# Optimization experiments

Measured on AMD Instinct MI355X. Metric: run time of the kernel, lower is better.

## Reference

```python
import jax, jax.numpy as jnp
import numpy as np

B, S, C, H = 2, 4096, 640, 8
D = C // H  # head_dim = 80


def setup_inputs() -> dict:
    key = jax.random.key(0)
    ks = jax.random.split(key, 5)
    init = 0.02
    return {
        "hidden_states": jax.random.normal(ks[0], (B, S, C), dtype=jnp.float32),
        "Wq": jax.random.normal(ks[1], (C, C), dtype=jnp.float32) * init,
        "Wk": jax.random.normal(ks[2], (C, C), dtype=jnp.float32) * init,
        "Wv": jax.random.normal(ks[3], (C, C), dtype=jnp.float32) * init,
        "Wo": jax.random.normal(ks[4], (C, C), dtype=jnp.float32) * init,
        "bo": jnp.zeros((C,), dtype=jnp.float32),
    }


def reference(hidden_states, Wq, Wk, Wv, Wo, bo):
    # self-attention: encoder_hidden_states is None -> k,v from hidden_states
    x = hidden_states  # [B, S, C]
    q = jnp.einsum("bsc,cd->bsd", x, Wq)
    k = jnp.einsum("bsc,cd->bsd", x, Wk)
    v = jnp.einsum("bsc,cd->bsd", x, Wv)

    # head_to_batch_dim: [B, S, H*D] -> [B, H, S, D]
    def split_heads(t):
        return t.reshape(B, S, H, D).transpose(0, 2, 1, 3)

    q, k, v = split_heads(q), split_heads(k), split_heads(v)

    scale = 1.0 / jnp.sqrt(jnp.float32(D))
    # get_attention_scores: baddbmm(q, k^T) * scale, softmax over keys
    scores = jnp.einsum("bhqd,bhkd->bhqk", q, k) * scale  # [B, H, S, S]
    probs = jax.nn.softmax(scores, axis=-1)
    out = jnp.einsum("bhqk,bhkd->bhqd", probs, v)  # [B, H, S, D]

    # batch_to_head_dim + to_out[0] linear (Dropout is identity at eval)
    out = out.transpose(0, 2, 1, 3).reshape(B, S, C)
    out = jnp.einsum("bsc,cd->bsd", out, Wo) + bo
    # residual_connection=False, rescale_output_factor=1.0 (diffusers defaults)
    return out
```

## Files before the change

kernel.cpp:

```cpp
#include <hip/hip_runtime.h>
#include <hip/hip_bf16.h>

typedef __bf16 bf16x8 __attribute__((ext_vector_type(8)));
typedef float f32x4 __attribute__((ext_vector_type(4)));
typedef float f32x16 __attribute__((ext_vector_type(16)));
typedef unsigned short u16;
typedef unsigned int u32;
typedef u16 u16x8 __attribute__((ext_vector_type(8)));

#define DEV __device__ __forceinline__

DEV u16 f2b(float f) {
    u32 u = __builtin_bit_cast(u32, f);
    u32 r = (u + 0x7FFFu + ((u >> 16) & 1u)) >> 16;
    return (u16)r;
}
DEV bf16x8 load8(const u16* p) {
    return __builtin_bit_cast(bf16x8, *(const uint4*)p);
}
DEV u32 cvtpk(float lo, float hi) {
    u32 r;
    asm("v_cvt_pk_bf16_f32 %0, %1, %2" : "=v"(r) : "v"(lo), "v"(hi));
    return r;
}
DEV void gld_lds16(const u16* g, const char* l) {
    __builtin_amdgcn_global_load_lds(
        (const __attribute__((address_space(1))) u32*)(unsigned long long)g,
        (__attribute__((address_space(3))) u32*)(u32)(unsigned long long)l,
        16, 0, 0);
}

__global__ __launch_bounds__(256) void cvt_x(const float* __restrict__ X, u16* __restrict__ Xb) {
    long i = ((long)blockIdx.x * 256 + threadIdx.x) * 8;
    float fa[8];
    *(uint4*)fa = *(const uint4*)(X + i);
    *(uint4*)(fa + 4) = *(const uint4*)(X + i + 4);
    u16x8 t;
    #pragma unroll
    for (int j = 0; j < 8; ++j) t[j] = f2b(fa[j]);
    *(u16x8*)(Xb + i) = t;
}

__global__ __launch_bounds__(256) void cvt_w3(
    const float* __restrict__ Wq, const float* __restrict__ Wk, const float* __restrict__ Wv,
    u16* __restrict__ Wt3)
{
    const int z = blockIdx.z;
    const float* W = (z == 0) ? Wq : ((z == 1) ? Wk : Wv);
    u16* Wt = Wt3 + (long)z * 409600;
    const int k0 = blockIdx.x * 64, n0 = blockIdx.y * 64;
    const int t = threadIdx.x;
    __shared__ u16 T[64][72];
    {
        int kl = t >> 2, nc = (t & 3) * 16;
        const float* src = W + (long)(k0 + kl) * 640 + n0 + nc;
        float fa[16];
        #pragma unroll
        for (int i = 0; i < 4; ++i) *(uint4*)(fa + i * 4) = *(const uint4*)(src + i * 4);
        #pragma unroll
        for (int j = 0; j < 16; ++j) T[nc + j][kl] = f2b(fa[j]);
    }
    __syncthreads();
    {
        int nl = t >> 2, kc = (t & 3) * 16;
        u16* dst = Wt + (long)(n0 + nl) * 640 + k0 + kc;
        *(uint4*)dst = *(const uint4*)&T[nl][kc];
        *(uint4*)(dst + 8) = *(const uint4*)&T[nl][kc + 8];
    }
}
__global__ __launch_bounds__(256) void cvt_w1(const float* __restrict__ W, u16* __restrict__ Wt) {
    const int k0 = blockIdx.x * 64, n0 = blockIdx.y * 64;
    const int t = threadIdx.x;
    __shared__ u16 T[64][72];
    {
        int kl = t >> 2, nc = (t & 3) * 16;
        const float* src = W + (long)(k0 + kl) * 640 + n0 + nc;
        float fa[16];
        #pragma unroll
        for (int i = 0; i < 4; ++i) *(uint4*)(fa + i * 4) = *(const uint4*)(src + i * 4);
        #pragma unroll
        for (int j = 0; j < 16; ++j) T[nc + j][kl] = f2b(fa[j]);
    }
    __syncthreads();
    {
        int nl = t >> 2, kc = (t & 3) * 16;
        u16* dst = Wt + (long)(n0 + nl) * 640 + k0 + kc;
        *(uint4*)dst = *(const uint4*)&T[nl][kc];
        *(uint4*)(dst + 8) = *(const uint4*)&T[nl][kc + 8];
    }
}

#define GEMM_CORE(A_PTR, BT_PTR)                                                  \
    const int tid = threadIdx.x;                                                  \
    const int lane = tid & 63;                                                    \
    const int w = tid >> 6;                                                       \
    const int wm = w >> 1, wn = w & 1;                                            \
    const int lg = lane >> 4, lr = lane & 15;                                     \
    __shared__ __align__(16) char Bb[2][16384];                                   \
    auto stage = [&](int kt0, int buf) {                                          \
        _Pragma("unroll")                                                         \
        for (int i = 0; i < 4; ++i) {                                             \
            int c = i * 256 + tid;                                                \
            int n = c >> 3, cc = c & 7;                                           \
            gld_lds16(BT_PTR + (long)(n0 + n) * 640 + kt0 + ((cc ^ (n & 7)) * 8), \
                      Bb[buf] + (c & ~63) * 16);                                  \
        }                                                                         \
    };                                                                            \
    f32x4 acc[4][4] = {};                                                         \
    stage(0, 0);                                                                  \
    for (int t = 0; t < 10; ++t) {                                                \
        __syncthreads();                                                          \
        if (t < 9) stage((t + 1) * 64, (t + 1) & 1);                              \
        const char* Bc = Bb[t & 1];                                               \
        _Pragma("unroll")                                                         \
        for (int ks = 0; ks < 64; ks += 32) {                                     \
            bf16x8 a[4], b[4];                                                    \
            _Pragma("unroll")                                                     \
            for (int mi = 0; mi < 4; ++mi) {                                      \
                int row = m0 + wm * 64 + mi * 16 + lr;                            \
                a[mi] = load8(A_PTR + (long)row * 640 + t * 64 + ks + lg * 8);    \
            }                                                                     \
            _Pragma("unroll")                                                     \
            for (int ni = 0; ni < 4; ++ni) {                                      \
                int n = wn * 64 + ni * 16 + lr;                                   \
                int cc = (ks >> 3) + lg;                                          \
                b[ni] = __builtin_bit_cast(bf16x8,                                \
                    *(const uint4*)(Bc + (n * 8 + (cc ^ (n & 7))) * 16));         \
            }                                                                     \
            _Pragma("unroll")                                                     \
            for (int mi = 0; mi < 4; ++mi)                                        \
                _Pragma("unroll")                                                 \
                for (int ni = 0; ni < 4; ++ni)                                    \
                    acc[mi][ni] = __builtin_amdgcn_mfma_f32_16x16x32_bf16(        \
                        a[mi], b[ni], acc[mi][ni], 0, 0, 0);                      \
        }                                                                         \
    }

__global__ __launch_bounds__(256, 3) void gemm_qkv(
    const u16* __restrict__ X, const u16* __restrict__ Wt3,
    u16* __restrict__ q_ws, u16* __restrict__ k_ws, u16* __restrict__ v_ws)
{
    const int z = blockIdx.z;
    const u16* Wt = Wt3 + (long)z * 409600;
    const int m0 = blockIdx.x * 128;
    const int n0 = blockIdx.y * 128;
    GEMM_CORE(X, Wt)
    #pragma unroll
    for (int mi = 0; mi < 4; ++mi)
        #pragma unroll
        for (int ni = 0; ni < 4; ++ni)
            #pragma unroll
            for (int r = 0; r < 4; ++r) {
                int m = m0 + wm * 64 + mi * 16 + lg * 4 + r;
                int n = n0 + wn * 64 + ni * 16 + lr;
                int b_ = m >> 12, s = m & 4095;
                int h = n / 80, d = n % 80;
                long bh = b_ * 8 + h;
                int tt = s >> 6, jj = s & 63;
                float val = acc[mi][ni][r];
                if (z == 0) {
                    q_ws[(bh * 4096 + s) * 80 + d] = f2b(val * 0.16131517891624225f);
                } else if (z == 1) {
                    k_ws[(bh * 64 + tt) * 5120 + (((d >> 4) * 2 + ((d >> 3) & 1)) * 64 + jj) * 8 + (d & 7)] = f2b(val);
                } else {
                    int kb = jj >> 5, h2 = (jj >> 4) & 1, hv = (jj >> 2) & 1;
                    int jv = ((jj >> 3) & 1) * 4 + (jj & 3);
                    int c = kb * 2 + h2;
                    u16* vt = v_ws + (bh * 64 + tt) * 6144;
                    vt[((c * 2 + hv) * 96 + d) * 8 + jv] = f2b(val);
                    if (d == 0) vt[((c * 2 + hv) * 96 + 80) * 8 + jv] = 0x3F80;
                }
            }
}

__global__ __launch_bounds__(256, 3) void gemm_out(
    const u16* __restrict__ X, const u16* __restrict__ Wt,
    const float* __restrict__ bias, float* __restrict__ out)
{
    const int m0 = blockIdx.x * 128;
    const int n0 = blockIdx.y * 128;
    GEMM_CORE(X, Wt)
    #pragma unroll
    for (int mi = 0; mi < 4; ++mi)
        #pragma unroll
        for (int ni = 0; ni < 4; ++ni)
            #pragma unroll
            for (int r = 0; r < 4; ++r) {
                int m = m0 + wm * 64 + mi * 16 + lg * 4 + r;
                int n = n0 + wn * 64 + ni * 16 + lr;
                out[(long)m * 640 + n] = acc[mi][ni][r] + bias[n];
            }
}

__global__ __launch_bounds__(256, 2) void attn(
    const u16* __restrict__ q_ws, const u16* __restrict__ k_ws,
    const u16* __restrict__ v_ws, u16* __restrict__ o_ws)
{
    const int l = blockIdx.x;
    const int xcd = l & 7, inner = l >> 3;
    const int bh = (xcd << 1) | (inner >> 5);
    const int qx = inner & 31;
    const int qb = qx * 128;
    const int tid = threadIdx.x;
    const int lane = tid & 63;
    const int w = tid >> 6;
    const int hi = lane >> 5;
    const int lq = lane & 31;

    __shared__ __align__(16) char Kb[2][10240];
    __shared__ __align__(16) char Vb[2][12288];

    const u16* ktile = k_ws + (long)bh * 64 * 5120;
    const u16* vtile = v_ws + (long)bh * 64 * 6144;

    bf16x8 qf[5];
    const int qrow = qb + w * 32 + lq;
    #pragma unroll
    for (int kc = 0; kc < 5; ++kc)
        qf[kc] = load8(q_ws + ((long)bh * 4096 + qrow) * 80 + kc * 16 + hi * 8);

    f32x16 acc[3] = {};

    auto stage = [&](int t, int buf) {
        const u16* kt_ = ktile + (long)t * 5120;
        const u16* vt_ = vtile + (long)t * 6144;
        #pragma unroll
        for (int i = 0; i < 6; ++i) {
            int c = i * 256 + tid;
            if (c < 1408) {
                int cw = c & ~63;
                if (cw < 640) gld_lds16(kt_ + (long)c * 8, Kb[buf] + cw * 16);
                else          gld_lds16(vt_ + (long)(c - 640) * 8, Vb[buf] + (cw - 640) * 16);
            }
        }
    };

    stage(0, 0);
    for (int t = 0; t < 64; ++t) {
        __syncthreads();
        if (t < 63) stage(t + 1, (t + 1) & 1);
        const char* Kc = Kb[t & 1];
        const char* Vc = Vb[t & 1];

        f32x16 sf[2] = {};
        __builtin_amdgcn_s_setprio(1);
        #pragma unroll
        for (int kc = 0; kc < 5; ++kc) {
            #pragma unroll
            for (int kb = 0; kb < 2; ++kb) {
                bf16x8 kf = __builtin_bit_cast(bf16x8,
                    *(const uint4*)(Kc + ((kc * 2 + hi) * 64 + kb * 32 + lq) * 16));
                sf[kb] = __builtin_amdgcn_mfma_f32_32x32x16_bf16(kf, qf[kc], sf[kb], 0, 0, 0);
            }
        }
        __builtin_amdgcn_s_setprio(0);

        #pragma unroll
        for (int kb = 0; kb < 2; ++kb)
            #pragma unroll
            for (int r = 0; r < 16; ++r)
                sf[kb][r] = __builtin_amdgcn_exp2f(sf[kb][r]);

        bf16x8 pa[4];
        #pragma unroll
        for (int kb = 0; kb < 2; ++kb)
            #pragma unroll
            for (int h = 0; h < 2; ++h) {
                uint4 wv;
                wv.x = cvtpk(sf[kb][h * 8 + 0], sf[kb][h * 8 + 1]);
                wv.y = cvtpk(sf[kb][h * 8 + 2], sf[kb][h * 8 + 3]);
                wv.z = cvtpk(sf[kb][h * 8 + 4], sf[kb][h * 8 + 5]);
                wv.w = cvtpk(sf[kb][h * 8 + 6], sf[kb][h * 8 + 7]);
                pa[kb * 2 + h] = __builtin_bit_cast(bf16x8, wv);
            }

        __builtin_amdgcn_s_setprio(1);
        #pragma unroll
        for (int db = 0; db < 3; ++db)
            #pragma unroll
            for (int c = 0; c < 4; ++c) {
                bf16x8 vf = __builtin_bit_cast(bf16x8,
                    *(const uint4*)(Vc + ((c * 2 + hi) * 96 + db * 32 + lq) * 16));
                acc[db] = __builtin_amdgcn_mfma_f32_32x32x16_bf16(pa[c], vf, acc[db], 0, 0, 0);
            }
        __builtin_amdgcn_s_setprio(0);
    }

    const int b_ = bh >> 3, h8 = bh & 7;
    #pragma unroll
    for (int r = 0; r < 16; ++r) {
        int ql = (r & 3) + 8 * (r >> 2) + 4 * hi;
        float lsum = __shfl(acc[2][r], (hi << 5) + 16);
        float inv = 1.0f / lsum;
        int row = qb + w * 32 + ql;
        #pragma unroll
        for (int db = 0; db < 3; ++db) {
            int d = db * 32 + lq;
            if (d < 80)
                o_ws[((long)b_ * 4096 + row) * 640 + h8 * 80 + d] = f2b(acc[db][r] * inv);
        }
    }
}

extern "C" void kernel_launch(void* const* d_in, const int* in_sizes, int n_in,
                              void* d_out, int out_size, void* d_ws, size_t ws_size,
                              hipStream_t stream) {
    const float* x  = (const float*)d_in[0];
    const float* Wq = (const float*)d_in[1];
    const float* Wk = (const float*)d_in[2];
    const float* Wv = (const float*)d_in[3];
    const float* Wo = (const float*)d_in[4];
    const float* bo = (const float*)d_in[5];

    u16* ws = (u16*)d_ws;
    const long SZ = 5242880;
    u16* Xb   = ws;
    u16* q_ws = ws + SZ;
    u16* k_ws = ws + 2 * SZ;
    u16* v_ws = ws + 3 * SZ;
    u16* Wt3  = ws + 3 * SZ + 6291456;
    u16* o_ws = Xb;
    u16* WtO  = k_ws;

    cvt_x<<<2560, 256, 0, stream>>>(x, Xb);
    dim3 gw3(10, 10, 3);
    cvt_w3<<<gw3, 256, 0, stream>>>(Wq, Wk, Wv, Wt3);
    hipMemsetAsync(v_ws, 0, 6291456 * sizeof(u16), stream);

    dim3 g1(64, 5, 3);
    gemm_qkv<<<g1, 256, 0, stream>>>(Xb, Wt3, q_ws, k_ws, v_ws);

    attn<<<512, 256, 0, stream>>>(q_ws, k_ws, v_ws, o_ws);

    dim3 gw1(10, 10);
    cvt_w1<<<gw1, 256, 0, stream>>>(Wo, WtO);
    dim3 g3(64, 5);
    gemm_out<<<g3, 256, 0, stream>>>(o_ws, WtO, bo, (float*)d_out);
}
```

Measured before the change: 202.6 us.

## Load attention K tiles straight into register double buffers, drop V memset

```diff
diff --git a/kernel.cpp b/kernel.cpp
--- a/kernel.cpp
+++ b/kernel.cpp
@@ -207,7 +207,6 @@
     const int hi = lane >> 5;
     const int lq = lane & 31;
 
-    __shared__ __align__(16) char Kb[2][10240];
     __shared__ __align__(16) char Vb[2][12288];
 
     const u16* ktile = k_ws + (long)bh * 64 * 5120;
@@ -221,46 +220,36 @@
 
     f32x16 acc[3] = {};
 
-    auto stage = [&](int t, int buf) {
-        const u16* kt_ = ktile + (long)t * 5120;
+    auto stage_v = [&](int t, int buf) {
         const u16* vt_ = vtile + (long)t * 6144;
         #pragma unroll
-        for (int i = 0; i < 6; ++i) {
+        for (int i = 0; i < 3; ++i) {
             int c = i * 256 + tid;
-            if (c < 1408) {
-                int cw = c & ~63;
-                if (cw < 640) gld_lds16(kt_ + (long)c * 8, Kb[buf] + cw * 16);
-                else          gld_lds16(vt_ + (long)(c - 640) * 8, Vb[buf] + (cw - 640) * 16);
-            }
+            gld_lds16(vt_ + (long)c * 8, Vb[buf] + (c & ~63) * 16);
         }
     };
-
-    stage(0, 0);
-    for (int t = 0; t < 64; ++t) {
-        __syncthreads();
-        if (t < 63) stage(t + 1, (t + 1) & 1);
-        const char* Kc = Kb[t & 1];
-        const char* Vc = Vb[t & 1];
-
+    auto loadK = [&](int t, bf16x8* kr) {
+        const u16* kt_ = ktile + (long)t * 5120;
+        #pragma unroll
+        for (int kc = 0; kc < 5; ++kc)
+            #pragma unroll
+            for (int kb = 0; kb < 2; ++kb)
+                kr[kc * 2 + kb] = load8(kt_ + (((kc * 2 + hi) * 64) + kb * 32 + lq) * 8);
+    };
+    auto compute = [&](const bf16x8* kr, const char* Vc) {
         f32x16 sf[2] = {};
         __builtin_amdgcn_s_setprio(1);
         #pragma unroll
-        for (int kc = 0; kc < 5; ++kc) {
-            #pragma unroll
-            for (int kb = 0; kb < 2; ++kb) {
-                bf16x8 kf = __builtin_bit_cast(bf16x8,
-                    *(const uint4*)(Kc + ((kc * 2 + hi) * 64 + kb * 32 + lq) * 16));
-                sf[kb] = __builtin_amdgcn_mfma_f32_32x32x16_bf16(kf, qf[kc], sf[kb], 0, 0, 0);
-            }
-        }
+        for (int kc = 0; kc < 5; ++kc)
+            #pragma unroll
+            for (int kb = 0; kb < 2; ++kb)
+                sf[kb] = __builtin_amdgcn_mfma_f32_32x32x16_bf16(kr[kc * 2 + kb], qf[kc], sf[kb], 0, 0, 0);
         __builtin_amdgcn_s_setprio(0);
-
         #pragma unroll
         for (int kb = 0; kb < 2; ++kb)
             #pragma unroll
             for (int r = 0; r < 16; ++r)
                 sf[kb][r] = __builtin_amdgcn_exp2f(sf[kb][r]);
-
         bf16x8 pa[4];
         #pragma unroll
         for (int kb = 0; kb < 2; ++kb)
@@ -273,17 +262,30 @@
                 wv.w = cvtpk(sf[kb][h * 8 + 6], sf[kb][h * 8 + 7]);
                 pa[kb * 2 + h] = __builtin_bit_cast(bf16x8, wv);
             }
-
         __builtin_amdgcn_s_setprio(1);
         #pragma unroll
         for (int db = 0; db < 3; ++db)
             #pragma unroll
-            for (int c = 0; c < 4; ++c) {
+            for (int cc = 0; cc < 4; ++cc) {
                 bf16x8 vf = __builtin_bit_cast(bf16x8,
-                    *(const uint4*)(Vc + ((c * 2 + hi) * 96 + db * 32 + lq) * 16));
-                acc[db] = __builtin_amdgcn_mfma_f32_32x32x16_bf16(pa[c], vf, acc[db], 0, 0, 0);
+                    *(const uint4*)(Vc + ((cc * 2 + hi) * 96 + db * 32 + lq) * 16));
+                acc[db] = __builtin_amdgcn_mfma_f32_32x32x16_bf16(pa[cc], vf, acc[db], 0, 0, 0);
             }
         __builtin_amdgcn_s_setprio(0);
+    };
+
+    bf16x8 kA[10], kB[10];
+    loadK(0, kA);
+    stage_v(0, 0);
+    for (int t = 0; t < 64; t += 2) {
+        __syncthreads();
+        if (t < 63) stage_v(t + 1, (t + 1) & 1);
+        loadK(t + 1, kB);
+        compute(kA, Vb[t & 1]);
+        __syncthreads();
+        if (t + 1 < 63) stage_v(t + 2, t & 1);
+        loadK(t + 2 < 64 ? t + 2 : 0, kA);
+        compute(kB, Vb[(t + 1) & 1]);
     }
 
     const int b_ = bh >> 3, h8 = bh & 7;
@@ -325,7 +327,6 @@
     cvt_x<<<2560, 256, 0, stream>>>(x, Xb);
     dim3 gw3(10, 10, 3);
     cvt_w3<<<gw3, 256, 0, stream>>>(Wq, Wk, Wv, Wt3);
-    hipMemsetAsync(v_ws, 0, 6291456 * sizeof(u16), stream);
 
     dim3 g1(64, 5, 3);
     gemm_qkv<<<g1, 256, 0, stream>>>(Xb, Wt3, q_ws, k_ws, v_ws);
```

New measurement: 201.7 us. Within noise of the previous version (-0.5%).
